# Performance work log

Hardware: AMD Instinct MI355X
Metric: run time of the kernel (lower is better)

Reference implementation:

```python
import jax, jax.numpy as jnp
import numpy as np

B, C, CI, H, W = 16, 256, 128, 64, 64


def setup_inputs() -> dict:
    key = jax.random.key(0)
    k1, k2, k3, k4, k5, k6 = jax.random.split(key, 6)
    x_gallery = jax.random.normal(k1, (B, C, H, W), dtype=jnp.float32)
    x_query = jax.random.normal(k2, (B, C, H, W), dtype=jnp.float32)
    # 1x1 conv weights (kernel_size=1 -> equivalent to per-pixel linear map)
    s = 1.0 / np.sqrt(C)
    theta_w = jax.random.uniform(k3, (CI, C), jnp.float32, -s, s)
    theta_b = jax.random.uniform(k4, (CI,), jnp.float32, -s, s)
    phi_w = jax.random.uniform(k5, (CI, C), jnp.float32, -s, s)
    phi_b = jax.random.uniform(k6, (CI,), jnp.float32, -s, s)
    return {"x_gallery": x_gallery, "x_query": x_query,
            "theta_w": theta_w, "theta_b": theta_b,
            "phi_w": phi_w, "phi_b": phi_b}


def reference(x_gallery, x_query, theta_w, theta_b, phi_w, phi_b):
    b, c, h, w = x_gallery.shape
    # 1x1 convs == channel-mixing einsum
    theta_x = jnp.einsum('bchw,oc->bohw', x_gallery, theta_w) + theta_b[None, :, None, None]
    phi_x = jnp.einsum('bchw,oc->bohw', x_query, phi_w) + phi_b[None, :, None, None]
    t = theta_x.reshape(b, theta_x.shape[1], -1)   # [B, CI, HW]
    p = phi_x.reshape(b, phi_x.shape[1], -1)       # [B, CI, H'W']
    n = p.shape[-1]
    # f[b, i, j] = <theta[:, i], phi[:, j]> / N   (norm == 'size')
    f = jnp.einsum('bci,bcj->bij', t, p) / n       # [B, HW, H'W']
    f = jnp.max(f, axis=2)                         # row-wise max (non-softmax attention)
    f = f.reshape(b, 1, h, w)
    return jax.nn.sigmoid(f)                       # message == 'attention_map'
```

## Files before the change

kernel.cpp:

```cpp
#include <hip/hip_runtime.h>
#include <hip/hip_bf16.h>

#define B_   16
#define CIN  256
#define CO   128
#define HW   4096

typedef __attribute__((ext_vector_type(8))) short short8;
typedef __attribute__((ext_vector_type(4))) float f32x4;

__device__ __forceinline__ short f32_to_bf16_rne(float f) {
    union { float f; unsigned u; } v; v.f = f;
    unsigned u = v.u;
    u += 0x7fffu + ((u >> 16) & 1u);
    return (short)(u >> 16);
}

__global__ __launch_bounds__(256) void wconv_kernel(
    const float* __restrict__ tw, const float* __restrict__ pw,
    short* __restrict__ wbf)
{
    const int idx = blockIdx.x * 256 + threadIdx.x;
    const float v = (idx < CO * CIN) ? tw[idx] : pw[idx - CO * CIN];
    wbf[idx] = f32_to_bf16_rne(v);
}

__global__ __launch_bounds__(256, 3) void proj_kernel(
    const float* __restrict__ xg, const float* __restrict__ xq,
    const float* __restrict__ tb, const float* __restrict__ pb,
    const short* __restrict__ wbf,
    short* __restrict__ tT, short* __restrict__ pT)
{
    const int n     = blockIdx.x;
    const int xcd   = n & 7;
    const int q     = n >> 3;
    const int b     = xcd + 8 * (q & 1);
    const int r2    = q >> 1;
    const int which = r2 & 1;
    const int itile = r2 >> 1;

    const float* x    = which ? xq : xg;
    const float* bias = which ? pb : tb;
    const short* wb   = wbf + which * CO * CIN;
    short*       out  = which ? pT : tT;

    const int i0   = itile * 64;
    const int tid  = threadIdx.x;
    const int lane = tid & 63;
    const int wv   = tid >> 6;
    const int nrow = lane & 15;
    const int quad = lane >> 4;

    const int col4 = tid & 15;
    const int rp   = tid >> 4;

    __shared__ short xT[2][64][72];

    f32x4 acc[4][2] = {};

    float bias_v[2];
    bias_v[0] = bias[wv * 32 + 0  + nrow];
    bias_v[1] = bias[wv * 32 + 16 + nrow];

    short8 wfrag[4][2][2];
    #pragma unroll
    for (int c4 = 0; c4 < 4; c4++)
        #pragma unroll
        for (int ks = 0; ks < 2; ks++)
            #pragma unroll
            for (int nt = 0; nt < 2; nt++)
                wfrag[c4][ks][nt] = *(const short8*)(
                    wb + (wv * 32 + nt * 16 + nrow) * CIN + c4 * 64 + ks * 32 + quad * 8);

    const float* xb = x + (long)b * CIN * HW + i0;

    float4 cva[2], cvb[2];

    auto load_chunk = [&](int cc) {
        #pragma unroll
        for (int rr = 0; rr < 2; rr++) {
            const int row = rr * 32 + rp * 2;
            cva[rr] = *(const float4*)(xb + (long)(cc + row)     * HW + col4 * 4);
            cvb[rr] = *(const float4*)(xb + (long)(cc + row + 1) * HW + col4 * 4);
        }
    };
    auto store_chunk = [&](int buf) {
        #pragma unroll
        for (int rr = 0; rr < 2; rr++) {
            const int row = rr * 32 + rp * 2;
            const float* pa  = (const float*)&cva[rr];
            const float* pb2 = (const float*)&cvb[rr];
            #pragma unroll
            for (int k = 0; k < 4; k++) {
                const unsigned lo = (unsigned short)f32_to_bf16_rne(pa[k]);
                const unsigned hi = (unsigned short)f32_to_bf16_rne(pb2[k]);
                *(unsigned*)&xT[buf][col4 * 4 + k][row] = lo | (hi << 16);
            }
        }
    };
    auto mfma_chunk = [&](int c4, int buf) {
        #pragma unroll
        for (int ks = 0; ks < 2; ks++)
            #pragma unroll
            for (int mt = 0; mt < 4; mt++) {
                const short8 a = *(const short8*)&xT[buf][mt * 16 + nrow][ks * 32 + quad * 8];
                acc[mt][0] = __builtin_amdgcn_mfma_f32_16x16x32_bf16(a, wfrag[c4][ks][0], acc[mt][0], 0, 0, 0);
                acc[mt][1] = __builtin_amdgcn_mfma_f32_16x16x32_bf16(a, wfrag[c4][ks][1], acc[mt][1], 0, 0, 0);
            }
    };

    load_chunk(0);
    store_chunk(0);
    #pragma unroll
    for (int c4 = 0; c4 < 4; c4++) {
        __syncthreads();
        if (c4 < 3) load_chunk(c4 * 64 + 64);
        mfma_chunk(c4, c4 & 1);
        if (c4 < 3) store_chunk((c4 + 1) & 1);
    }

    #pragma unroll
    for (int mt = 0; mt < 4; mt++)
        #pragma unroll
        for (int nt = 0; nt < 2; nt++) {
            const int co = wv * 32 + nt * 16 + nrow;
            #pragma unroll
            for (int r = 0; r < 4; r++) {
                const int il = mt * 16 + quad * 4 + r;
                out[((long)b * HW + i0 + il) * CO + co] =
                    f32_to_bf16_rne(acc[mt][nt][r] + bias_v[nt]);
            }
        }
}

__global__ __launch_bounds__(256, 1) void maxgemm_kernel(
    const short* __restrict__ tT, const short* __restrict__ pT,
    float* __restrict__ out)
{
    const int n     = blockIdx.x;
    const int b     = (n & 7) + 8 * ((n >> 3) & 1);
    const int itile = n >> 4;
    const int i0    = itile * 256;
    const int tid   = threadIdx.x;
    const int lane  = tid & 63;
    const int wv    = tid >> 6;
    const int nrow  = lane & 15;
    const int quad  = lane >> 4;

    __shared__ short bT[2][64][128];

    short8 afrag[4][4];
    {
        const short* tb2 = tT + ((long)b * HW + i0 + wv * 64) * CO;
        #pragma unroll
        for (int mt = 0; mt < 4; mt++)
            #pragma unroll
            for (int ks = 0; ks < 4; ks++)
                afrag[mt][ks] = *(const short8*)(tb2 + (mt * 16 + nrow) * CO + ks * 32 + quad * 8);
    }

    const short* pb2 = pT + (long)b * HW * CO;
    const int sc8 = tid & 15;
    const int sj0 = tid >> 4;

    short8 sreg[4];
    auto stage_load = [&](int jt) {
        const short* src = pb2 + (long)jt * 64 * CO;
        #pragma unroll
        for (int r = 0; r < 4; r++)
            sreg[r] = *(const short8*)(src + (sj0 + r * 16) * CO + sc8 * 8);
    };
    auto stage_write = [&](int buf) {
        #pragma unroll
        for (int r = 0; r < 4; r++) {
            const int j  = sj0 + r * 16;
            const int c8 = sc8 ^ (j & 7);
            *(short8*)&bT[buf][j][c8 * 8] = sreg[r];
        }
    };

    f32x4 vmax[4];
    #pragma unroll
    for (int mt = 0; mt < 4; mt++)
        vmax[mt] = (f32x4){-1e30f, -1e30f, -1e30f, -1e30f};

    auto compute = [&](int buf) {
        #pragma unroll
        for (int nt = 0; nt < 4; nt++) {
            short8 bf[4];
            const int j = nt * 16 + nrow;
            #pragma unroll
            for (int ks = 0; ks < 4; ks++) {
                const int c8 = (ks * 4 + quad) ^ (j & 7);
                bf[ks] = *(const short8*)&bT[buf][j][c8 * 8];
            }
            #pragma unroll
            for (int mt = 0; mt < 4; mt++) {
                f32x4 acc = {0.f, 0.f, 0.f, 0.f};
                #pragma unroll
                for (int ks = 0; ks < 4; ks++)
                    acc = __builtin_amdgcn_mfma_f32_16x16x32_bf16(afrag[mt][ks], bf[ks], acc, 0, 0, 0);
                #pragma unroll
                for (int r = 0; r < 4; r++)
                    vmax[mt][r] = fmaxf(vmax[mt][r], acc[r]);
            }
        }
    };

    stage_load(0);
    stage_write(0);
    for (int jt = 0; jt < 64; jt++) {
        __syncthreads();
        if (jt < 63) stage_load(jt + 1);
        compute(jt & 1);
        if (jt < 63) stage_write((jt + 1) & 1);
    }

    #pragma unroll
    for (int mt = 0; mt < 4; mt++)
        #pragma unroll
        for (int r = 0; r < 4; r++) {
            float v = vmax[mt][r];
            #pragma unroll
            for (int m = 8; m >= 1; m >>= 1)
                v = fmaxf(v, __shfl_xor(v, m, 64));
            vmax[mt][r] = v;
        }

    if (nrow == 0) {
        #pragma unroll
        for (int mt = 0; mt < 4; mt++)
            #pragma unroll
            for (int r = 0; r < 4; r++) {
                const float v = vmax[mt][r] * (1.0f / (float)HW);
                out[(long)b * HW + i0 + wv * 64 + mt * 16 + quad * 4 + r] =
                    1.0f / (1.0f + __expf(-v));
            }
    }
}

extern "C" void kernel_launch(void* const* d_in, const int* in_sizes, int n_in,
                              void* d_out, int out_size, void* d_ws, size_t ws_size,
                              hipStream_t stream) {
    const float* xg = (const float*)d_in[0];
    const float* xq = (const float*)d_in[1];
    const float* tw = (const float*)d_in[2];
    const float* tb = (const float*)d_in[3];
    const float* pw = (const float*)d_in[4];
    const float* pb = (const float*)d_in[5];
    float* out = (float*)d_out;

    short* tT  = (short*)d_ws;
    short* pT  = tT + (size_t)B_ * HW * CO;
    short* wbf = pT + (size_t)B_ * HW * CO;

    wconv_kernel<<<(2 * CO * CIN) / 256, 256, 0, stream>>>(tw, pw, wbf);
    proj_kernel<<<B_ * (HW / 64) * 2, 256, 0, stream>>>(xg, xq, tb, pb, wbf, tT, pT);
    maxgemm_kernel<<<B_ * (HW / 256), 256, 0, stream>>>(tT, pT, out);
}
```

Before: 250.5 us.

## Load phi fragments directly from global into registers, dropping LDS staging

Measured after the change: 299.5 us. +19.5%, slower.

```diff
diff --git a/kernel.cpp b/kernel.cpp
--- a/kernel.cpp
+++ b/kernel.cpp
@@ -147,8 +147,6 @@
     const int nrow  = lane & 15;
     const int quad  = lane >> 4;
 
-    __shared__ short bT[2][64][128];
-
     short8 afrag[4][4];
     {
         const short* tb2 = tT + ((long)b * HW + i0 + wv * 64) * CO;
@@ -159,61 +157,45 @@
                 afrag[mt][ks] = *(const short8*)(tb2 + (mt * 16 + nrow) * CO + ks * 32 + quad * 8);
     }
 
-    const short* pb2 = pT + (long)b * HW * CO;
-    const int sc8 = tid & 15;
-    const int sj0 = tid >> 4;
-
-    short8 sreg[4];
-    auto stage_load = [&](int jt) {
-        const short* src = pb2 + (long)jt * 64 * CO;
-        #pragma unroll
-        for (int r = 0; r < 4; r++)
-            sreg[r] = *(const short8*)(src + (sj0 + r * 16) * CO + sc8 * 8);
-    };
-    auto stage_write = [&](int buf) {
-        #pragma unroll
-        for (int r = 0; r < 4; r++) {
-            const int j  = sj0 + r * 16;
-            const int c8 = sc8 ^ (j & 7);
-            *(short8*)&bT[buf][j][c8 * 8] = sreg[r];
-        }
-    };
+    const short* pbase = pT + (long)b * HW * CO + (long)nrow * CO + quad * 8;
 
     f32x4 vmax[4];
     #pragma unroll
     for (int mt = 0; mt < 4; mt++)
         vmax[mt] = (f32x4){-1e30f, -1e30f, -1e30f, -1e30f};
 
-    auto compute = [&](int buf) {
-        #pragma unroll
-        for (int nt = 0; nt < 4; nt++) {
-            short8 bf[4];
-            const int j = nt * 16 + nrow;
+    short8 bf0[2][4], bf1[2][4];
+
+    auto load_tile = [&](int jt, short8 (*dst)[4]) {
+        const short* p2 = pbase + (long)jt * 32 * CO;
+        #pragma unroll
+        for (int nt = 0; nt < 2; nt++)
+            #pragma unroll
+            for (int ks = 0; ks < 4; ks++)
+                dst[nt][ks] = *(const short8*)(p2 + nt * 16 * CO + ks * 32);
+    };
+    auto compute = [&](short8 (*bf)[4]) {
+        #pragma unroll
+        for (int mt = 0; mt < 4; mt++) {
+            f32x4 acc0 = {0.f, 0.f, 0.f, 0.f};
+            f32x4 acc1 = {0.f, 0.f, 0.f, 0.f};
             #pragma unroll
             for (int ks = 0; ks < 4; ks++) {
-                const int c8 = (ks * 4 + quad) ^ (j & 7);
-                bf[ks] = *(const short8*)&bT[buf][j][c8 * 8];
-            }
-            #pragma unroll
-            for (int mt = 0; mt < 4; mt++) {
-                f32x4 acc = {0.f, 0.f, 0.f, 0.f};
-                #pragma unroll
-                for (int ks = 0; ks < 4; ks++)
-                    acc = __builtin_amdgcn_mfma_f32_16x16x32_bf16(afrag[mt][ks], bf[ks], acc, 0, 0, 0);
-                #pragma unroll
-                for (int r = 0; r < 4; r++)
-                    vmax[mt][r] = fmaxf(vmax[mt][r], acc[r]);
-            }
-        }
-    };
-
-    stage_load(0);
-    stage_write(0);
-    for (int jt = 0; jt < 64; jt++) {
-        __syncthreads();
-        if (jt < 63) stage_load(jt + 1);
-        compute(jt & 1);
-        if (jt < 63) stage_write((jt + 1) & 1);
+                acc0 = __builtin_amdgcn_mfma_f32_16x16x32_bf16(afrag[mt][ks], bf[0][ks], acc0, 0, 0, 0);
+                acc1 = __builtin_amdgcn_mfma_f32_16x16x32_bf16(afrag[mt][ks], bf[1][ks], acc1, 0, 0, 0);
+            }
+            #pragma unroll
+            for (int r = 0; r < 4; r++)
+                vmax[mt][r] = fmaxf(vmax[mt][r], fmaxf(acc0[r], acc1[r]));
+        }
+    };
+
+    load_tile(0, bf0);
+    for (int jt = 0; jt < 128; jt += 2) {
+        load_tile(jt + 1, bf1);
+        compute(bf0);
+        load_tile((jt + 2 < 128) ? jt + 2 : 0, bf0);
+        compute(bf1);
     }
 
     #pragma unroll
```

## Split maxgemm work across waves by column tile and halve row tile per block

Applied to the files above, without the earlier changes.

Result: slower. 269.9 us (+7.8%).

```diff
diff --git a/kernel.cpp b/kernel.cpp
--- a/kernel.cpp
+++ b/kernel.cpp
@@ -133,14 +133,16 @@
         }
 }
 
-__global__ __launch_bounds__(256, 1) void maxgemm_kernel(
+__global__ __launch_bounds__(256, 2) void maxgemm_kernel(
     const short* __restrict__ tT, const short* __restrict__ pT,
     float* __restrict__ out)
 {
     const int n     = blockIdx.x;
-    const int b     = (n & 7) + 8 * ((n >> 3) & 1);
-    const int itile = n >> 4;
-    const int i0    = itile * 256;
+    const int xcd   = n & 7;
+    const int q     = n >> 3;
+    const int b     = xcd + 8 * (q & 1);
+    const int itile = q >> 1;
+    const int i0    = itile * 128;
     const int tid   = threadIdx.x;
     const int lane  = tid & 63;
     const int wv    = tid >> 6;
@@ -148,24 +150,25 @@
     const int quad  = lane >> 4;
 
     __shared__ short bT[2][64][128];
-
-    short8 afrag[4][4];
+    __shared__ float smax[128][4];
+
+    short8 afrag[8][4];
     {
-        const short* tb2 = tT + ((long)b * HW + i0 + wv * 64) * CO;
-        #pragma unroll
-        for (int mt = 0; mt < 4; mt++)
+        const short* tb2 = tT + ((long)b * HW + i0) * CO;
+        #pragma unroll
+        for (int mt = 0; mt < 8; mt++)
             #pragma unroll
             for (int ks = 0; ks < 4; ks++)
                 afrag[mt][ks] = *(const short8*)(tb2 + (mt * 16 + nrow) * CO + ks * 32 + quad * 8);
     }
 
-    const short* pb2 = pT + (long)b * HW * CO;
+    const short* pbb = pT + (long)b * HW * CO;
     const int sc8 = tid & 15;
     const int sj0 = tid >> 4;
 
     short8 sreg[4];
     auto stage_load = [&](int jt) {
-        const short* src = pb2 + (long)jt * 64 * CO;
+        const short* src = pbb + (long)jt * 64 * CO;
         #pragma unroll
         for (int r = 0; r < 4; r++)
             sreg[r] = *(const short8*)(src + (sj0 + r * 16) * CO + sc8 * 8);
@@ -179,31 +182,28 @@
         }
     };
 
-    f32x4 vmax[4];
-    #pragma unroll
-    for (int mt = 0; mt < 4; mt++)
+    f32x4 vmax[8];
+    #pragma unroll
+    for (int mt = 0; mt < 8; mt++)
         vmax[mt] = (f32x4){-1e30f, -1e30f, -1e30f, -1e30f};
 
     auto compute = [&](int buf) {
-        #pragma unroll
-        for (int nt = 0; nt < 4; nt++) {
-            short8 bf[4];
-            const int j = nt * 16 + nrow;
-            #pragma unroll
-            for (int ks = 0; ks < 4; ks++) {
-                const int c8 = (ks * 4 + quad) ^ (j & 7);
-                bf[ks] = *(const short8*)&bT[buf][j][c8 * 8];
-            }
-            #pragma unroll
-            for (int mt = 0; mt < 4; mt++) {
-                f32x4 acc = {0.f, 0.f, 0.f, 0.f};
-                #pragma unroll
-                for (int ks = 0; ks < 4; ks++)
-                    acc = __builtin_amdgcn_mfma_f32_16x16x32_bf16(afrag[mt][ks], bf[ks], acc, 0, 0, 0);
-                #pragma unroll
-                for (int r = 0; r < 4; r++)
-                    vmax[mt][r] = fmaxf(vmax[mt][r], acc[r]);
-            }
+        short8 bf[4];
+        const int j = wv * 16 + nrow;
+        #pragma unroll
+        for (int ks = 0; ks < 4; ks++) {
+            const int c8 = (ks * 4 + quad) ^ (j & 7);
+            bf[ks] = *(const short8*)&bT[buf][j][c8 * 8];
+        }
+        #pragma unroll
+        for (int mt = 0; mt < 8; mt++) {
+            f32x4 acc = {0.f, 0.f, 0.f, 0.f};
+            #pragma unroll
+            for (int ks = 0; ks < 4; ks++)
+                acc = __builtin_amdgcn_mfma_f32_16x16x32_bf16(afrag[mt][ks], bf[ks], acc, 0, 0, 0);
+            #pragma unroll
+            for (int r = 0; r < 4; r++)
+                vmax[mt][r] = fmaxf(vmax[mt][r], acc[r]);
         }
     };
 
@@ -217,7 +217,7 @@
     }
 
     #pragma unroll
-    for (int mt = 0; mt < 4; mt++)
+    for (int mt = 0; mt < 8; mt++)
         #pragma unroll
         for (int r = 0; r < 4; r++) {
             float v = vmax[mt][r];
@@ -229,13 +229,18 @@
 
     if (nrow == 0) {
         #pragma unroll
-        for (int mt = 0; mt < 4; mt++)
-            #pragma unroll
-            for (int r = 0; r < 4; r++) {
-                const float v = vmax[mt][r] * (1.0f / (float)HW);
-                out[(long)b * HW + i0 + wv * 64 + mt * 16 + quad * 4 + r] =
-                    1.0f / (1.0f + __expf(-v));
-            }
+        for (int mt = 0; mt < 8; mt++)
+            #pragma unroll
+            for (int r = 0; r < 4; r++)
+                smax[mt * 16 + quad * 4 + r][wv] = vmax[mt][r];
+    }
+    __syncthreads();
+
+    if (tid < 128) {
+        float v = fmaxf(fmaxf(smax[tid][0], smax[tid][1]),
+                        fmaxf(smax[tid][2], smax[tid][3]));
+        v *= (1.0f / (float)HW);
+        out[(long)b * HW + i0 + tid] = 1.0f / (1.0f + __expf(-v));
     }
 }
 
@@ -256,5 +261,5 @@
 
     wconv_kernel<<<(2 * CO * CIN) / 256, 256, 0, stream>>>(tw, pw, wbf);
     proj_kernel<<<B_ * (HW / 64) * 2, 256, 0, stream>>>(xg, xq, tb, pb, wbf, tT, pT);
-    maxgemm_kernel<<<B_ * (HW / 256), 256, 0, stream>>>(tT, pT, out);
-}
+    maxgemm_kernel<<<B_ * (HW / 128), 256, 0, stream>>>(tT, pT, out);
+}
```
